# Kernel tuning notes

Measured on AMD Instinct MI355X. Metric: run time of the kernel, lower is better.

Reference implementation:

```python
import jax, jax.numpy as jnp
import numpy as np


def _splat_sum(x, flow):
    # Bilinear forward-splatting scatter-add ('summation' mode of the splatting package).
    # x: [B, C, M, N] values; flow: [B, 2, M, N], flow[:,0]=dx (cols/x), flow[:,1]=dy (rows/y).
    B, C, M, N = x.shape
    gy, gx = jnp.meshgrid(jnp.arange(M, dtype=x.dtype), jnp.arange(N, dtype=x.dtype), indexing='ij')
    fx = gx[None] + flow[:, 0]  # [B, M, N] target x coordinate
    fy = gy[None] + flow[:, 1]  # [B, M, N] target y coordinate
    x0 = jnp.floor(fx)
    y0 = jnp.floor(fy)
    src = x.transpose(0, 2, 3, 1).reshape(B, M * N, C)  # [B, MN, C]
    out = jnp.zeros((B, M * N, C), dtype=x.dtype)
    bidx = jnp.arange(B)[:, None]
    for dx in (0.0, 1.0):
        for dy in (0.0, 1.0):
            xi = x0 + dx
            yi = y0 + dy
            # bilinear weight of this corner
            w = (1.0 - jnp.abs(fx - xi)) * (1.0 - jnp.abs(fy - yi))
            valid = (xi >= 0) & (xi <= N - 1) & (yi >= 0) & (yi <= M - 1)
            xi_i = jnp.clip(xi, 0, N - 1).astype(jnp.int32)
            yi_i = jnp.clip(yi, 0, M - 1).astype(jnp.int32)
            lin = (yi_i * N + xi_i).reshape(B, M * N)
            wv = jnp.where(valid, w, 0.0).reshape(B, M * N, 1)
            out = out.at[bidx, lin].add(src * wv)
    return out.reshape(B, M, N, C).transpose(0, 3, 1, 2)


def setup_inputs() -> dict:
    key = jax.random.key(0)
    k1, k2, k3 = jax.random.split(key, 3)
    B, T, M, N = 8, 12, 384, 384
    x_re = jax.random.normal(k1, (B, T, M, N), dtype=jnp.float32)
    x_im = jax.random.normal(k2, (B, T, M, N), dtype=jnp.float32)
    u = jax.random.normal(k3, (B, T, M, N, 2), dtype=jnp.float32)
    return {"x_re": x_re, "x_im": x_im, "u": u}


def reference(x_re, x_im, u):
    B, T, M, N, _ = u.shape
    # real/imag splatted with identical flow -> fuse as 2 channels of one splat
    xr = x_re.reshape(-1, M, N)
    xi = x_im.reshape(-1, M, N)
    x = jnp.stack([xr, xi], axis=1)  # [B*T, 2, M, N]
    flow = u.reshape(-1, M, N, 2).transpose(0, 3, 1, 2)  # [B*T, 2, M, N]
    out = _splat_sum(x, flow)
    out_re = out[:, 0].reshape(B, T, M, N)
    out_im = out[:, 1].reshape(B, T, M, N)
    # torch.complex(...) then sum over axis -3 (the T/motion-state axis)
    return jax.lax.complex(out_re, out_im).sum(axis=-3)
```

## Files before the change

kernel.cpp:

```cpp
#include <hip/hip_runtime.h>


#define BB   8
#define TT   12
#define MM   384
#define NN   384
#define TS   32
#define HALO 8
#define LW   (TS + 2*HALO)
#define TCH  6
#define NTX  (NN/TS)
#define NTY  (MM/TS)
#define TILES (NTX*NTY)

template<bool CPLX>
__global__ __launch_bounds__(256)
void splat_kernel(const float* __restrict__ xr, const float* __restrict__ xi,
                  const float* __restrict__ u, float* __restrict__ out)
{
    constexpr int ROWW = CPLX ? (2 * LW + 2) : (LW + 1);
    __shared__ float tile[LW * ROWW];
    for (int i = threadIdx.x; i < LW * ROWW; i += 256) tile[i] = 0.0f;
    __syncthreads();

    const int blk   = blockIdx.x;
    const int tilei = blk % TILES;
    const int tx    = tilei % NTX;
    const int ty    = tilei / NTX;
    const int bt    = blk / TILES;
    const int tc    = bt & 1;
    const int b     = bt >> 1;
    const int n0    = tx * TS;
    const int m0    = ty * TS;

    const int lrow = threadIdx.x >> 3;
    const int lc4  = (threadIdx.x & 7) << 2;
    const int gm   = m0 + lrow;
    const int gn   = n0 + lc4;

    for (int tt = 0; tt < TCH; ++tt) {
        const int t = tc * TCH + tt;
        const size_t base = ((size_t)((b * TT + t) * MM + gm)) * NN + gn;
        const float4 vr = *reinterpret_cast<const float4*>(xr + base);
        float4 vi = make_float4(0.f, 0.f, 0.f, 0.f);
        if (CPLX) vi = *reinterpret_cast<const float4*>(xi + base);
        const float4 ua = *reinterpret_cast<const float4*>(u + 2 * base);
        const float4 ub = *reinterpret_cast<const float4*>(u + 2 * base + 4);
        const float re[4]  = {vr.x, vr.y, vr.z, vr.w};
        const float im[4]  = {vi.x, vi.y, vi.z, vi.w};
        const float dxs[4] = {ua.x, ua.z, ub.x, ub.z};
        const float dys[4] = {ua.y, ua.w, ub.y, ub.w};
        #pragma unroll
        for (int j = 0; j < 4; ++j) {
            const float fx = (float)(gn + j) + dxs[j];
            const float fy = (float)gm + dys[j];
            const float x0f = floorf(fx);
            const float y0f = floorf(fy);
            const int   x0  = (int)x0f;
            const int   y0  = (int)y0f;
            const float frx = fx - x0f;
            const float fry = fy - y0f;
            const float wx[2] = {1.0f - frx, frx};
            const float wy[2] = {1.0f - fry, fry};
            #pragma unroll
            for (int cy = 0; cy < 2; ++cy) {
                const int yc = y0 + cy;
                if ((unsigned)yc >= (unsigned)MM) continue;
                #pragma unroll
                for (int cx = 0; cx < 2; ++cx) {
                    const int xc = x0 + cx;
                    if ((unsigned)xc >= (unsigned)NN) continue;
                    const float w  = wx[cx] * wy[cy];
                    const int  lr  = yc - (m0 - HALO);
                    const int  lc  = xc - (n0 - HALO);
                    if ((unsigned)lr < (unsigned)LW && (unsigned)lc < (unsigned)LW) {
                        if (CPLX) {
                            float* p = &tile[lr * ROWW + lc * 2];
                            atomicAdd(p,     w * re[j]);
                            atomicAdd(p + 1, w * im[j]);
                        } else {
                            atomicAdd(&tile[lr * ROWW + lc], w * re[j]);
                        }
                    } else {
                        if (CPLX) {
                            float* q = out + (((size_t)b * MM + yc) * NN + xc) * 2;
                            unsafeAtomicAdd(q,     w * re[j]);
                            unsafeAtomicAdd(q + 1, w * im[j]);
                        } else {
                            unsafeAtomicAdd(out + ((size_t)b * MM + yc) * NN + xc,
                                            w * re[j]);
                        }
                    }
                }
            }
        }
    }
    __syncthreads();

    for (int i = threadIdx.x; i < LW * LW; i += 256) {
        const int lr = i / LW;
        const int lc = i - lr * LW;
        const int gy = m0 - HALO + lr;
        const int gx = n0 - HALO + lc;
        if ((unsigned)gy < (unsigned)MM && (unsigned)gx < (unsigned)NN) {
            if (CPLX) {
                const float vre = tile[lr * ROWW + lc * 2];
                const float vim = tile[lr * ROWW + lc * 2 + 1];
                if (vre != 0.0f || vim != 0.0f) {
                    float* q = out + (((size_t)b * MM + gy) * NN + gx) * 2;
                    unsafeAtomicAdd(q,     vre);
                    unsafeAtomicAdd(q + 1, vim);
                }
            } else {
                const float v = tile[lr * ROWW + lc];
                if (v != 0.0f)
                    unsafeAtomicAdd(out + ((size_t)b * MM + gy) * NN + gx, v);
            }
        }
    }
}

extern "C" void kernel_launch(void* const* d_in, const int* in_sizes, int n_in,
                              void* d_out, int out_size, void* d_ws, size_t ws_size,
                              hipStream_t stream) {
    const float* xr = (const float*)d_in[0];
    const float* xi = (const float*)d_in[1];
    const float* u  = (const float*)d_in[2];
    float* out = (float*)d_out;

    hipMemsetAsync(d_out, 0, (size_t)out_size * sizeof(float), stream);

    const int grid = BB * (TT / TCH) * TILES;
    const bool cplx = (out_size >= 2 * BB * MM * NN);
    if (cplx)
        splat_kernel<true ><<<grid, 256, 0, stream>>>(xr, xi, u, out);
    else
        splat_kernel<false><<<grid, 256, 0, stream>>>(xr, xi, u, out);
}
```

Before: 449.1 us.

## Replace tile flush atomics with workspace dump and gather-reduce second pass

Result: slower. 486.3 us (+8.3%).

```diff
diff --git a/kernel.cpp b/kernel.cpp
--- a/kernel.cpp
+++ b/kernel.cpp
@@ -8,17 +8,18 @@
 #define TS   32
 #define HALO 8
 #define LW   (TS + 2*HALO)
-#define TCH  6
 #define NTX  (NN/TS)
 #define NTY  (MM/TS)
 #define TILES (NTX*NTY)
 
-template<bool CPLX>
+template<bool CPLX, bool USE_WS>
 __global__ __launch_bounds__(256)
-void splat_kernel(const float* __restrict__ xr, const float* __restrict__ xi,
-                  const float* __restrict__ u, float* __restrict__ out)
+void splat_phase1(const float* __restrict__ xr, const float* __restrict__ xi,
+                  const float* __restrict__ u, float* __restrict__ out,
+                  float* __restrict__ ws)
 {
     constexpr int ROWW = CPLX ? (2 * LW + 2) : (LW + 1);
+    constexpr int ELEMS = CPLX ? (LW * LW * 2) : (LW * LW);
     __shared__ float tile[LW * ROWW];
     for (int i = threadIdx.x; i < LW * ROWW; i += 256) tile[i] = 0.0f;
     __syncthreads();
@@ -27,9 +28,7 @@
     const int tilei = blk % TILES;
     const int tx    = tilei % NTX;
     const int ty    = tilei / NTX;
-    const int bt    = blk / TILES;
-    const int tc    = bt & 1;
-    const int b     = bt >> 1;
+    const int b     = blk / TILES;
     const int n0    = tx * TS;
     const int m0    = ty * TS;
 
@@ -38,8 +37,7 @@
     const int gm   = m0 + lrow;
     const int gn   = n0 + lc4;
 
-    for (int tt = 0; tt < TCH; ++tt) {
-        const int t = tc * TCH + tt;
+    for (int t = 0; t < TT; ++t) {
         const size_t base = ((size_t)((b * TT + t) * MM + gm)) * NN + gn;
         const float4 vr = *reinterpret_cast<const float4*>(xr + base);
         float4 vi = make_float4(0.f, 0.f, 0.f, 0.f);
@@ -97,26 +95,86 @@
     }
     __syncthreads();
 
-    for (int i = threadIdx.x; i < LW * LW; i += 256) {
-        const int lr = i / LW;
-        const int lc = i - lr * LW;
-        const int gy = m0 - HALO + lr;
-        const int gx = n0 - HALO + lc;
-        if ((unsigned)gy < (unsigned)MM && (unsigned)gx < (unsigned)NN) {
+    if (USE_WS) {
+        float* dst = ws + (size_t)blk * ELEMS;
+        for (int i = threadIdx.x; i < ELEMS; i += 256) {
             if (CPLX) {
-                const float vre = tile[lr * ROWW + lc * 2];
-                const float vim = tile[lr * ROWW + lc * 2 + 1];
-                if (vre != 0.0f || vim != 0.0f) {
-                    float* q = out + (((size_t)b * MM + gy) * NN + gx) * 2;
-                    unsafeAtomicAdd(q,     vre);
-                    unsafeAtomicAdd(q + 1, vim);
+                const int pix  = i >> 1;
+                const int comp = i & 1;
+                dst[i] = tile[(pix / LW) * ROWW + (pix % LW) * 2 + comp];
+            } else {
+                dst[i] = tile[(i / LW) * ROWW + (i % LW)];
+            }
+        }
+    } else {
+        for (int i = threadIdx.x; i < LW * LW; i += 256) {
+            const int lr = i / LW;
+            const int lc = i - lr * LW;
+            const int gy = m0 - HALO + lr;
+            const int gx = n0 - HALO + lc;
+            if ((unsigned)gy < (unsigned)MM && (unsigned)gx < (unsigned)NN) {
+                if (CPLX) {
+                    const float vre = tile[lr * ROWW + lc * 2];
+                    const float vim = tile[lr * ROWW + lc * 2 + 1];
+                    if (vre != 0.0f || vim != 0.0f) {
+                        float* q = out + (((size_t)b * MM + gy) * NN + gx) * 2;
+                        unsafeAtomicAdd(q,     vre);
+                        unsafeAtomicAdd(q + 1, vim);
+                    }
+                } else {
+                    const float v = tile[lr * ROWW + lc];
+                    if (v != 0.0f)
+                        unsafeAtomicAdd(out + ((size_t)b * MM + gy) * NN + gx, v);
                 }
+            }
+        }
+    }
+}
+
+template<bool CPLX>
+__global__ __launch_bounds__(256)
+void splat_phase2(const float* __restrict__ ws, float* __restrict__ out)
+{
+    constexpr int ELEMS = CPLX ? (LW * LW * 2) : (LW * LW);
+    const int idx = blockIdx.x * 256 + threadIdx.x;
+    const int b   = idx / (MM * NN);
+    const int rem = idx - b * (MM * NN);
+    const int y   = rem / NN;
+    const int x   = rem - y * NN;
+
+    const int ty0 = y >> 5, ry = y & 31;
+    const int tx0 = x >> 5, rx = x & 31;
+
+    int tys[2]; int nty = 0;
+    tys[nty++] = ty0;
+    if (ry < HALO      && ty0 > 0)       tys[nty++] = ty0 - 1;
+    if (ry >= TS-HALO  && ty0 < NTY-1)   tys[nty++] = ty0 + 1;
+    int txs[2]; int ntx = 0;
+    txs[ntx++] = tx0;
+    if (rx < HALO      && tx0 > 0)       txs[ntx++] = tx0 - 1;
+    if (rx >= TS-HALO  && tx0 < NTX-1)   txs[ntx++] = tx0 + 1;
+
+    float sre = 0.0f, sim = 0.0f;
+    for (int a = 0; a < nty; ++a) {
+        const int ty = tys[a];
+        const int lr = y - (ty * TS - HALO);
+        for (int c = 0; c < ntx; ++c) {
+            const int tx = txs[c];
+            const int lc = x - (tx * TS - HALO);
+            const float* src = ws + ((size_t)(b * TILES + ty * NTX + tx)) * ELEMS;
+            if (CPLX) {
+                sre += src[(lr * LW + lc) * 2];
+                sim += src[(lr * LW + lc) * 2 + 1];
             } else {
-                const float v = tile[lr * ROWW + lc];
-                if (v != 0.0f)
-                    unsafeAtomicAdd(out + ((size_t)b * MM + gy) * NN + gx, v);
-            }
-        }
+                sre += src[lr * LW + lc];
+            }
+        }
+    }
+    if (CPLX) {
+        out[2 * idx]     += sre;
+        out[2 * idx + 1] += sim;
+    } else {
+        out[idx] += sre;
     }
 }
 
@@ -127,13 +185,27 @@
     const float* xi = (const float*)d_in[1];
     const float* u  = (const float*)d_in[2];
     float* out = (float*)d_out;
+    float* ws  = (float*)d_ws;
 
     hipMemsetAsync(d_out, 0, (size_t)out_size * sizeof(float), stream);
 
-    const int grid = BB * (TT / TCH) * TILES;
     const bool cplx = (out_size >= 2 * BB * MM * NN);
-    if (cplx)
-        splat_kernel<true ><<<grid, 256, 0, stream>>>(xr, xi, u, out);
-    else
-        splat_kernel<false><<<grid, 256, 0, stream>>>(xr, xi, u, out);
+    const int  grid1 = BB * TILES;
+    const int  grid2 = (BB * MM * NN) / 256;
+    const size_t need = (size_t)grid1 * LW * LW * (cplx ? 2 : 1) * sizeof(float);
+
+    if (ws_size >= need) {
+        if (cplx) {
+            splat_phase1<true , true ><<<grid1, 256, 0, stream>>>(xr, xi, u, out, ws);
+            splat_phase2<true ><<<grid2, 256, 0, stream>>>(ws, out);
+        } else {
+            splat_phase1<false, true ><<<grid1, 256, 0, stream>>>(xr, xi, u, out, ws);
+            splat_phase2<false><<<grid2, 256, 0, stream>>>(ws, out);
+        }
+    } else {
+        if (cplx)
+            splat_phase1<true , false><<<grid1, 256, 0, stream>>>(xr, xi, u, out, ws);
+        else
+            splat_phase1<false, false><<<grid1, 256, 0, stream>>>(xr, xi, u, out, ws);
+    }
 }
```
